# Kernel optimization log

Hardware: AMD Instinct MI355X
Metric: run time of the kernel (lower is better)

Reference implementation:

```python
import jax, jax.numpy as jnp
import numpy as np

N_NODES = 50000
N_EDGES = 800000
IN_DIM = 128
HID = 256
OUT_DIM = 256
N_HEADS = 8
E_DIM = 64
KV_IN = 2 * IN_DIM + E_DIM  # 320


def _mlp_params(key, din, dhid, dout):
    k1, k2 = jax.random.split(key)
    s1 = 1.0 / np.sqrt(din)
    s2 = 1.0 / np.sqrt(dhid)
    return (jax.random.uniform(k1, (din, dhid), jnp.float32, -s1, s1),
            jnp.zeros((dhid,), jnp.float32),
            jax.random.uniform(k2, (dhid, dout), jnp.float32, -s2, s2),
            jnp.zeros((dout,), jnp.float32))


def setup_inputs() -> dict:
    key = jax.random.key(0)
    kh, ke, kidx, kk, kv, kq = jax.random.split(key, 6)
    h = jax.random.normal(kh, (N_NODES, IN_DIM), jnp.float32)
    e = jax.random.normal(ke, (N_EDGES, E_DIM), jnp.float32)
    edge_index = jax.random.randint(kidx, (2, N_EDGES), 0, N_NODES, jnp.int64)
    Wk1, bk1, Wk2, bk2 = _mlp_params(kk, KV_IN, HID, OUT_DIM)
    Wv1, bv1, Wv2, bv2 = _mlp_params(kv, KV_IN, HID, OUT_DIM)
    Wq1, bq1, Wq2, bq2 = _mlp_params(kq, IN_DIM, HID, OUT_DIM)
    return {"h": h, "e": e, "edge_index": edge_index,
            "Wk1": Wk1, "bk1": bk1, "Wk2": Wk2, "bk2": bk2,
            "Wv1": Wv1, "bv1": bv1, "Wv2": Wv2, "bv2": bv2,
            "Wq1": Wq1, "bq1": bq1, "Wq2": Wq2, "bq2": bq2}


def _mlp(x, W1, b1, W2, b2):
    # MLP(in, out, hidden, norm=False): Linear -> ReLU -> Linear
    return jax.nn.relu(x @ W1 + b1) @ W2 + b2


def reference(h, e, edge_index,
              Wk1, bk1, Wk2, bk2,
              Wv1, bv1, Wv2, bv2,
              Wq1, bq1, Wq2, bq2):
    N = h.shape[0]
    d_head = OUT_DIM // N_HEADS
    src, dst = edge_index[0], edge_index[1]
    # gather endpoints: hi = h[dst], hj = h[src]
    kv_input = jnp.concatenate([e, h[dst], h[src]], axis=-1)  # [E, KV_IN]
    k = _mlp(kv_input, Wk1, bk1, Wk2, bk2).reshape(-1, N_HEADS, d_head)
    v = _mlp(kv_input, Wv1, bv1, Wv2, bv2).reshape(-1, N_HEADS, d_head)
    q = _mlp(h, Wq1, bq1, Wq2, bq2).reshape(-1, N_HEADS, d_head)
    # per-edge logits, scaled dot product [E, H]
    logits = jnp.sum(q[dst] * k, axis=-1) * (1.0 / np.sqrt(d_head))
    # scatter softmax over destination groups
    mx = jax.ops.segment_max(logits, dst, num_segments=N)  # [N, H]
    ex = jnp.exp(logits - mx[dst])
    den = jax.ops.segment_sum(ex, dst, num_segments=N)  # [N, H]
    alpha = ex / den[dst]  # [E, H]
    # weighted scatter-sum aggregate
    m = alpha[..., None] * v  # [E, H, d_head]
    out = jax.ops.segment_sum(m, dst, num_segments=N)  # [N, H, d_head]
    return out.reshape(N, OUT_DIM)
```

## Files before the change

### kernel.cpp

```cpp
#include <hip/hip_runtime.h>

#define NND 50000
#define NE  800000
#define IND 128
#define HD  256
#define OD  256
#define NH  8
#define ED  64
#define KVIN 320

typedef __attribute__((ext_vector_type(8))) short bf16x8;
typedef __attribute__((ext_vector_type(4))) float f32x4;

__device__ __forceinline__ float bf2f(unsigned short u) {
    union { unsigned int i; float f; } x; x.i = ((unsigned int)u) << 16; return x.f;
}
__device__ __forceinline__ unsigned short f2bf(float f) {
    union { float f; unsigned int i; } x; x.f = f;
    unsigned int u = x.i;
    u += 0x7FFFu + ((u >> 16) & 1u);
    return (unsigned short)(u >> 16);
}

__global__ void k_hist(const int* __restrict__ eidx, int* __restrict__ cnt) {
    int e = blockIdx.x * 256 + threadIdx.x;
    if (e < NE) atomicAdd(&cnt[eidx[NE + e]], 1);
}

__global__ __launch_bounds__(1024) void k_scan(const int* __restrict__ cnt,
                                               int* __restrict__ head) {
    __shared__ int part[1024];
    const int t = threadIdx.x;
    const int CH = (NND + 1023) / 1024;
    int base = t * CH;
    int s = 0;
    for (int i = 0; i < CH; ++i) { int idx = base + i; if (idx < NND) s += cnt[idx]; }
    part[t] = s;
    __syncthreads();
    for (int off = 1; off < 1024; off <<= 1) {
        int v = (t >= off) ? part[t - off] : 0;
        __syncthreads();
        part[t] += v;
        __syncthreads();
    }
    int excl = (t == 0) ? 0 : part[t - 1];
    for (int i = 0; i < CH; ++i) {
        int idx = base + i; if (idx >= NND) break;
        head[idx] = excl;
        excl += cnt[idx];
    }
}

__global__ void k_scatter(const int* __restrict__ eidx, int* __restrict__ head,
                          int* __restrict__ perm) {
    int e = blockIdx.x * 256 + threadIdx.x;
    if (e < NE) {
        int d = eidx[NE + e];
        int pos = atomicAdd(&head[d], 1);
        perm[pos] = e;
    }
}

__global__ void k_packw(const float* __restrict__ W, unsigned short* __restrict__ P,
                        int K, int N, int rowoff) {
    int tid = blockIdx.x * 256 + threadIdx.x;
    if (tid >= K * N) return;
    int j = tid & 7;
    int l = (tid >> 3) & 63;
    int rest = tid >> 9;
    int KS = K >> 5;
    int ks = rest % KS;
    int ct = rest / KS;
    int n = ct * 16 + (l & 15);
    int k = ks * 32 + (l >> 4) * 8 + j;
    P[tid] = f2bf(W[(size_t)(rowoff + k) * N + n]);
}

__global__ void k_h2bf(const float* __restrict__ h, unsigned short* __restrict__ hb, int n4) {
    int i = blockIdx.x * 256 + threadIdx.x;
    if (i < n4) {
        float4 v = *(const float4*)(h + (size_t)i * 4);
        ushort4 o;
        o.x = f2bf(v.x); o.y = f2bf(v.y); o.z = f2bf(v.z); o.w = f2bf(v.w);
        *(ushort4*)(hb + (size_t)i * 4) = o;
    }
}

__device__ __forceinline__ void zero_acc(f32x4 (&acc)[4][4]) {
    #pragma unroll
    for (int i = 0; i < 4; ++i)
        #pragma unroll
        for (int c = 0; c < 4; ++c)
            #pragma unroll
            for (int r = 0; r < 4; ++r) acc[i][c][r] = 0.f;
}

template<int KS, int STRIDE>
__device__ __forceinline__ void gemm_step(const unsigned short* A,
                                          const unsigned short* __restrict__ Wp,
                                          int w, int l, f32x4 (&acc)[4][4]) {
    for (int ks = 0; ks < KS; ++ks) {
        bf16x8 a[4], b[4];
        #pragma unroll
        for (int i = 0; i < 4; ++i)
            a[i] = *(const bf16x8*)(A + (i * 16 + (l & 15)) * STRIDE + ks * 32 + (l >> 4) * 8);
        #pragma unroll
        for (int c = 0; c < 4; ++c)
            b[c] = *(const bf16x8*)(Wp + (((4 * w + c) * KS + ks) * 64 + l) * 8);
        #pragma unroll
        for (int i = 0; i < 4; ++i)
            #pragma unroll
            for (int c = 0; c < 4; ++c)
                acc[i][c] = __builtin_amdgcn_mfma_f32_16x16x32_bf16(a[i], b[c], acc[i][c], 0, 0, 0);
    }
}

__global__ __launch_bounds__(256) void k_qmlp(
    const unsigned short* __restrict__ hb,
    const unsigned short* __restrict__ W1p, const float* __restrict__ b1,
    const unsigned short* __restrict__ W2p, const float* __restrict__ b2,
    unsigned short* __restrict__ qb)
{
    __shared__ unsigned short sX[64][136];
    __shared__ unsigned short sH[64][264];
    const int t = threadIdx.x, w = t >> 6, l = t & 63;
    const int m0 = blockIdx.x * 64;

    for (int c = t; c < 1024; c += 256) {
        int row = c >> 4, j = c & 15;
        int srcr = m0 + row; if (srcr >= NND) srcr = NND - 1;
        *(bf16x8*)(&sX[row][j * 8]) = *(const bf16x8*)(hb + (size_t)srcr * IND + j * 8);
    }
    __syncthreads();

    f32x4 acc[4][4];
    zero_acc(acc);
    gemm_step<4, 136>(&sX[0][0], W1p, w, l, acc);

    float bias1[4];
    #pragma unroll
    for (int c = 0; c < 4; ++c) bias1[c] = b1[64 * w + 16 * c + (l & 15)];
    #pragma unroll
    for (int i = 0; i < 4; ++i)
        #pragma unroll
        for (int c = 0; c < 4; ++c)
            #pragma unroll
            for (int r = 0; r < 4; ++r) {
                float v = acc[i][c][r] + bias1[c];
                v = v > 0.f ? v : 0.f;
                sH[i * 16 + (l >> 4) * 4 + r][64 * w + 16 * c + (l & 15)] = f2bf(v);
            }
    __syncthreads();

    zero_acc(acc);
    gemm_step<8, 264>(&sH[0][0], W2p, w, l, acc);

    float bias2[4];
    #pragma unroll
    for (int c = 0; c < 4; ++c) bias2[c] = b2[64 * w + 16 * c + (l & 15)];
    #pragma unroll
    for (int i = 0; i < 4; ++i)
        #pragma unroll
        for (int c = 0; c < 4; ++c)
            #pragma unroll
            for (int r = 0; r < 4; ++r) {
                int row = m0 + i * 16 + (l >> 4) * 4 + r;
                if (row < NND)
                    qb[(size_t)row * OD + 64 * w + 16 * c + (l & 15)] =
                        f2bf(acc[i][c][r] + bias2[c]);
            }
}

__global__ __launch_bounds__(256) void k_lin2(
    const unsigned short* __restrict__ hb,
    const unsigned short* __restrict__ Pd, const unsigned short* __restrict__ Ps,
    unsigned short* __restrict__ outd, unsigned short* __restrict__ outs)
{
    __shared__ unsigned short sX[64][136];
    const int t = threadIdx.x, w = t >> 6, l = t & 63;
    const int m0 = blockIdx.x * 64;

    for (int c = t; c < 1024; c += 256) {
        int row = c >> 4, j = c & 15;
        int srcr = m0 + row; if (srcr >= NND) srcr = NND - 1;
        *(bf16x8*)(&sX[row][j * 8]) = *(const bf16x8*)(hb + (size_t)srcr * IND + j * 8);
    }
    __syncthreads();

    f32x4 acc[4][4];
    zero_acc(acc);
    gemm_step<4, 136>(&sX[0][0], Pd, w, l, acc);
    #pragma unroll
    for (int i = 0; i < 4; ++i)
        #pragma unroll
        for (int c = 0; c < 4; ++c)
            #pragma unroll
            for (int r = 0; r < 4; ++r) {
                int row = m0 + i * 16 + (l >> 4) * 4 + r;
                if (row < NND)
                    outd[(size_t)row * HD + 64 * w + 16 * c + (l & 15)] = f2bf(acc[i][c][r]);
            }

    zero_acc(acc);
    gemm_step<4, 136>(&sX[0][0], Ps, w, l, acc);
    #pragma unroll
    for (int i = 0; i < 4; ++i)
        #pragma unroll
        for (int c = 0; c < 4; ++c)
            #pragma unroll
            for (int r = 0; r < 4; ++r) {
                int row = m0 + i * 16 + (l >> 4) * 4 + r;
                if (row < NND)
                    outs[(size_t)row * HD + 64 * w + 16 * c + (l & 15)] = f2bf(acc[i][c][r]);
            }
}

struct SmE {
    unsigned short E[64][72];
    unsigned short H[64][264];
    int   Eid[64];
    int   Src[64];
    int   Dst[64];
    float Ex[64][8];
};

__device__ __forceinline__ void stage_edges(SmE& sm, const float* __restrict__ eattr,
                                            const int* __restrict__ eidx,
                                            const int* __restrict__ perm,
                                            int e0, int t) {
    if (t < 64) {
        int eid = perm[e0 + t];
        sm.Eid[t] = eid;
        sm.Src[t] = eidx[eid];
        sm.Dst[t] = eidx[NE + eid];
    }
    __syncthreads();
    for (int c = t; c < 1024; c += 256) {
        int row = c >> 4, j = c & 15;
        float4 v = *(const float4*)(eattr + (size_t)sm.Eid[row] * ED + j * 4);
        ushort4 o; o.x = f2bf(v.x); o.y = f2bf(v.y); o.z = f2bf(v.z); o.w = f2bf(v.w);
        *(ushort4*)(&sm.E[row][j * 4]) = o;
    }
}

template<typename SM>
__device__ __forceinline__ void hidden_pass(SM& sm,
                                            const unsigned short* __restrict__ W1e,
                                            const float* __restrict__ b1,
                                            const unsigned short* __restrict__ ud,
                                            const unsigned short* __restrict__ us,
                                            int w, int l, int t, f32x4 (&acc)[4][4]) {
    zero_acc(acc);
    gemm_step<2, 72>(&sm.E[0][0], W1e, w, l, acc);
    float bias1[4];
    #pragma unroll
    for (int c = 0; c < 4; ++c) bias1[c] = b1[64 * w + 16 * c + (l & 15)];
    #pragma unroll
    for (int i = 0; i < 4; ++i)
        #pragma unroll
        for (int c = 0; c < 4; ++c)
            #pragma unroll
            for (int r = 0; r < 4; ++r)
                sm.H[i * 16 + (l >> 4) * 4 + r][64 * w + 16 * c + (l & 15)] =
                    f2bf(acc[i][c][r] + bias1[c]);
    __syncthreads();

    {
        int er = t >> 2;
        const unsigned short* udr = ud + (size_t)sm.Dst[er] * HD;
        const unsigned short* usr = us + (size_t)sm.Src[er] * HD;
        bf16x8 vd[8], vs[8];
        #pragma unroll
        for (int j = 0; j < 8; ++j) {
            int col = (j * 4 + (t & 3)) * 8;
            vd[j] = *(const bf16x8*)(udr + col);
            vs[j] = *(const bf16x8*)(usr + col);
        }
        #pragma unroll
        for (int j = 0; j < 8; ++j) {
            int col = (j * 4 + (t & 3)) * 8;
            bf16x8 hv = *(const bf16x8*)(&sm.H[er][col]);
            bf16x8 o;
            #pragma unroll
            for (int u = 0; u < 8; ++u) {
                float x = bf2f((unsigned short)hv[u]) + bf2f((unsigned short)vd[j][u])
                        + bf2f((unsigned short)vs[j][u]);
                o[u] = (short)f2bf(x > 0.f ? x : 0.f);
            }
            *(bf16x8*)(&sm.H[er][col]) = o;
        }
    }
    __syncthreads();
}

__global__ __launch_bounds__(256, 3) void k_edgeK(
    const float* __restrict__ eattr,
    const int* __restrict__ eidx, const int* __restrict__ perm,
    const unsigned short* __restrict__ W1e, const float* __restrict__ b1,
    const unsigned short* __restrict__ W2,  const float* __restrict__ b2,
    const unsigned short* __restrict__ ud,  const unsigned short* __restrict__ us,
    const unsigned short* __restrict__ qb,
    float* __restrict__ exbuf, float* __restrict__ den)
{
    __shared__ SmE sm;
    const int t = threadIdx.x, w = t >> 6, l = t & 63;
    const int e0 = blockIdx.x * 64;

    stage_edges(sm, eattr, eidx, perm, e0, t);
    __syncthreads();

    f32x4 acc[4][4];
    hidden_pass(sm, W1e, b1, ud, us, w, l, t, acc);

    zero_acc(acc);
    gemm_step<8, 264>(&sm.H[0][0], W2, w, l, acc);

    float bias2[4];
    #pragma unroll
    for (int c = 0; c < 4; ++c) bias2[c] = b2[64 * w + 16 * c + (l & 15)];
    __syncthreads();
    #pragma unroll
    for (int i = 0; i < 4; ++i)
        #pragma unroll
        for (int c = 0; c < 4; ++c)
            #pragma unroll
            for (int r = 0; r < 4; ++r)
                sm.H[i * 16 + (l >> 4) * 4 + r][64 * w + 16 * c + (l & 15)] =
                    f2bf(acc[i][c][r] + bias2[c]);
    __syncthreads();

    const float scale = 0.17677669529663687f;
    for (int p = t; p < 512; p += 256) {
        int er = p >> 3, hh = p & 7;
        int dn = sm.Dst[er];
        const unsigned short* qrow = qb + (size_t)dn * OD + hh * 32;
        float s = 0.f;
        #pragma unroll
        for (int jj = 0; jj < 32; jj += 8) {
            bf16x8 qv = *(const bf16x8*)(qrow + jj);
            bf16x8 kv = *(const bf16x8*)(&sm.H[er][hh * 32 + jj]);
            #pragma unroll
            for (int u = 0; u < 8; ++u)
                s += bf2f((unsigned short)qv[u]) * bf2f((unsigned short)kv[u]);
        }
        float ex = __expf(s * scale);
        exbuf[(size_t)(e0 + er) * NH + hh] = ex;
        sm.Ex[er][hh] = ex;
    }
    __syncthreads();
    if (t < NH) {
        float run = 0.f; int prev = sm.Dst[0];
        for (int er = 0; er < 64; ++er) {
            int dn = sm.Dst[er];
            if (dn != prev) { atomicAdd(&den[prev * NH + t], run); run = 0.f; prev = dn; }
            run += sm.Ex[er][t];
        }
        atomicAdd(&den[prev * NH + t], run);
    }
}

__global__ __launch_bounds__(256, 3) void k_edgeV(
    const float* __restrict__ eattr,
    const int* __restrict__ eidx, const int* __restrict__ perm,
    const unsigned short* __restrict__ W1e, const float* __restrict__ b1,
    const unsigned short* __restrict__ W2,  const float* __restrict__ b2,
    const unsigned short* __restrict__ ud,  const unsigned short* __restrict__ us,
    const float* __restrict__ exbuf, const float* __restrict__ den,
    float* __restrict__ outp)
{
    __shared__ SmE sm;
    const int t = threadIdx.x, w = t >> 6, l = t & 63;
    const int e0 = blockIdx.x * 64;

    stage_edges(sm, eattr, eidx, perm, e0, t);
    for (int p = t; p < 512; p += 256) {
        int er = p >> 3, hh = p & 7;
        sm.Ex[er][hh] = exbuf[(size_t)(e0 + er) * NH + hh] / den[sm.Dst[er] * NH + hh];
    }
    __syncthreads();

    f32x4 acc[4][4];
    hidden_pass(sm, W1e, b1, ud, us, w, l, t, acc);

    zero_acc(acc);
    gemm_step<8, 264>(&sm.H[0][0], W2, w, l, acc);

    float bias2[4];
    #pragma unroll
    for (int c = 0; c < 4; ++c) bias2[c] = b2[64 * w + 16 * c + (l & 15)];
    __syncthreads();
    #pragma unroll
    for (int i = 0; i < 4; ++i)
        #pragma unroll
        for (int c = 0; c < 4; ++c) {
            int col = 64 * w + 16 * c + (l & 15);
            int hh = col >> 5;
            #pragma unroll
            for (int r = 0; r < 4; ++r) {
                int er = i * 16 + (l >> 4) * 4 + r;
                sm.H[er][col] = f2bf((acc[i][c][r] + bias2[c]) * sm.Ex[er][hh]);
            }
        }
    __syncthreads();
    {
        float run = 0.f; int prev = sm.Dst[0];
        for (int er = 0; er < 64; ++er) {
            int dn = sm.Dst[er];
            if (dn != prev) {
                atomicAdd(outp + (size_t)prev * OD + t, run);
                run = 0.f; prev = dn;
            }
            run += bf2f(sm.H[er][t]);
        }
        atomicAdd(outp + (size_t)prev * OD + t, run);
    }
}

extern "C" void kernel_launch(void* const* d_in, const int* in_sizes, int n_in,
                              void* d_out, int out_size, void* d_ws, size_t ws_size,
                              hipStream_t stream)
{
    const float* h   = (const float*)d_in[0];
    const float* e   = (const float*)d_in[1];
    const int*   eid = (const int*)  d_in[2];
    const float* Wk1 = (const float*)d_in[3];
    const float* bk1 = (const float*)d_in[4];
    const float* Wk2 = (const float*)d_in[5];
    const float* bk2 = (const float*)d_in[6];
    const float* Wv1 = (const float*)d_in[7];
    const float* bv1 = (const float*)d_in[8];
    const float* Wv2 = (const float*)d_in[9];
    const float* bv2 = (const float*)d_in[10];
    const float* Wq1 = (const float*)d_in[11];
    const float* bq1 = (const float*)d_in[12];
    const float* Wq2 = (const float*)d_in[13];
    const float* bq2 = (const float*)d_in[14];

    char* ws = (char*)d_ws;
    unsigned short* hb   = (unsigned short*)(ws + 0);
    unsigned short* qb   = (unsigned short*)(ws + 12800000);
    unsigned short* udb  = (unsigned short*)(ws + 38400000);
    unsigned short* usb  = (unsigned short*)(ws + 64000000);
    float*          exb  = (float*)         (ws + 89600000);
    float*          den  = (float*)         (ws + 115200000);
    int*            cnt  = (int*)           (ws + 116800000);
    int*            head = (int*)           (ws + 117000000);
    int*            perm = (int*)           (ws + 117200000);
    unsigned short* Wq1p = (unsigned short*)(ws + 120400000);
    unsigned short* Wq2p = (unsigned short*)(ws + 120465536);
    unsigned short* WeK  = (unsigned short*)(ws + 120596608);
    unsigned short* W2K  = (unsigned short*)(ws + 120629376);
    unsigned short* WdK  = (unsigned short*)(ws + 120760448);
    unsigned short* WsK  = (unsigned short*)(ws + 120825984);
    unsigned short* WeV  = (unsigned short*)(ws + 120891520);
    unsigned short* W2V  = (unsigned short*)(ws + 120924288);
    unsigned short* WdV  = (unsigned short*)(ws + 121055360);
    unsigned short* WsV  = (unsigned short*)(ws + 121120896);
    const size_t needed = 121186432;
    if (ws_size < needed) return;

    hipMemsetAsync(d_out, 0, (size_t)NND * OD * sizeof(float), stream);
    hipMemsetAsync(den, 0, (size_t)NND * NH * sizeof(float), stream);
    hipMemsetAsync(cnt, 0, (size_t)NND * sizeof(int), stream);

    k_hist<<<(NE + 255) / 256, 256, 0, stream>>>(eid, cnt);
    k_scan<<<1, 1024, 0, stream>>>(cnt, head);
    k_scatter<<<(NE + 255) / 256, 256, 0, stream>>>(eid, head, perm);

    k_h2bf<<<(NND * IND / 4 + 255) / 256, 256, 0, stream>>>(h, hb, NND * IND / 4);

    k_packw<<<(IND * HD + 255) / 256, 256, 0, stream>>>(Wq1, Wq1p, IND, HD, 0);
    k_packw<<<(HD * OD + 255) / 256, 256, 0, stream>>>(Wq2, Wq2p, HD, OD, 0);
    k_packw<<<(ED * HD + 255) / 256, 256, 0, stream>>>(Wk1, WeK, ED, HD, 0);
    k_packw<<<(HD * OD + 255) / 256, 256, 0, stream>>>(Wk2, W2K, HD, OD, 0);
    k_packw<<<(IND * HD + 255) / 256, 256, 0, stream>>>(Wk1, WdK, IND, HD, 64);
    k_packw<<<(IND * HD + 255) / 256, 256, 0, stream>>>(Wk1, WsK, IND, HD, 192);
    k_packw<<<(ED * HD + 255) / 256, 256, 0, stream>>>(Wv1, WeV, ED, HD, 0);
    k_packw<<<(HD * OD + 255) / 256, 256, 0, stream>>>(Wv2, W2V, HD, OD, 0);
    k_packw<<<(IND * HD + 255) / 256, 256, 0, stream>>>(Wv1, WdV, IND, HD, 64);
    k_packw<<<(IND * HD + 255) / 256, 256, 0, stream>>>(Wv1, WsV, IND, HD, 192);

    k_qmlp<<<(NND + 63) / 64, 256, 0, stream>>>(hb, Wq1p, bq1, Wq2p, bq2, qb);

    k_lin2<<<(NND + 63) / 64, 256, 0, stream>>>(hb, WdK, WsK, udb, usb);
    k_edgeK<<<NE / 64, 256, 0, stream>>>(e, eid, perm, WeK, bk1, W2K, bk2,
                                         udb, usb, qb, exb, den);
    k_lin2<<<(NND + 63) / 64, 256, 0, stream>>>(hb, WdV, WsV, udb, usb);
    k_edgeV<<<NE / 64, 256, 0, stream>>>(e, eid, perm, WeV, bv1, W2V, bv2,
                                         udb, usb, exb, den, (float*)d_out);
}
```

Measured before the change: 921.7 us.

## Transpose MFMA operands so accumulators hold contiguous columns; fuse hidden epilogue gathers

Swaps the MFMA operand order so each lane's four accumulator values cover four consecutive output columns of one row. Epilogues can then pack bf16 pairs and use vector uint2 stores and float4 bias loads instead of scalar strided writes. The edge kernels' hidden layer no longer writes to shared memory, syncs, re-reads and adds the ud/us gathers in a separate pass. The gathered node projections are loaded straight into the first-layer epilogue registers, which removes one shared-memory round trip and one barrier. The cost is narrower global gathers (8-byte ushort4 per row instead of 16-byte bf16x8).

```diff
diff --git a/kernel.cpp b/kernel.cpp
--- a/kernel.cpp
+++ b/kernel.cpp
@@ -20,6 +20,9 @@
     unsigned int u = x.i;
     u += 0x7FFFu + ((u >> 16) & 1u);
     return (unsigned short)(u >> 16);
+}
+__device__ __forceinline__ unsigned int pk2(float a, float b) {
+    return (unsigned int)f2bf(a) | ((unsigned int)f2bf(b) << 16);
 }
 
 __global__ void k_hist(const int* __restrict__ eidx, int* __restrict__ cnt) {
@@ -88,30 +91,30 @@
 
 __device__ __forceinline__ void zero_acc(f32x4 (&acc)[4][4]) {
     #pragma unroll
-    for (int i = 0; i < 4; ++i)
+    for (int c = 0; c < 4; ++c)
+        #pragma unroll
+        for (int i = 0; i < 4; ++i)
+            #pragma unroll
+            for (int r = 0; r < 4; ++r) acc[c][i][r] = 0.f;
+}
+
+template<int KS, int STRIDE>
+__device__ __forceinline__ void gemmT(const unsigned short* X,
+                                      const unsigned short* __restrict__ Wp,
+                                      int w, int l, f32x4 (&acc)[4][4]) {
+    for (int ks = 0; ks < KS; ++ks) {
+        bf16x8 wf[4], xf[4];
+        #pragma unroll
+        for (int c = 0; c < 4; ++c)
+            wf[c] = *(const bf16x8*)(Wp + (((4 * w + c) * KS + ks) * 64 + l) * 8);
+        #pragma unroll
+        for (int i = 0; i < 4; ++i)
+            xf[i] = *(const bf16x8*)(X + (i * 16 + (l & 15)) * STRIDE + ks * 32 + (l >> 4) * 8);
         #pragma unroll
         for (int c = 0; c < 4; ++c)
             #pragma unroll
-            for (int r = 0; r < 4; ++r) acc[i][c][r] = 0.f;
-}
-
-template<int KS, int STRIDE>
-__device__ __forceinline__ void gemm_step(const unsigned short* A,
-                                          const unsigned short* __restrict__ Wp,
-                                          int w, int l, f32x4 (&acc)[4][4]) {
-    for (int ks = 0; ks < KS; ++ks) {
-        bf16x8 a[4], b[4];
-        #pragma unroll
-        for (int i = 0; i < 4; ++i)
-            a[i] = *(const bf16x8*)(A + (i * 16 + (l & 15)) * STRIDE + ks * 32 + (l >> 4) * 8);
-        #pragma unroll
-        for (int c = 0; c < 4; ++c)
-            b[c] = *(const bf16x8*)(Wp + (((4 * w + c) * KS + ks) * 64 + l) * 8);
-        #pragma unroll
-        for (int i = 0; i < 4; ++i)
-            #pragma unroll
-            for (int c = 0; c < 4; ++c)
-                acc[i][c] = __builtin_amdgcn_mfma_f32_16x16x32_bf16(a[i], b[c], acc[i][c], 0, 0, 0);
+            for (int i = 0; i < 4; ++i)
+                acc[c][i] = __builtin_amdgcn_mfma_f32_16x16x32_bf16(wf[c], xf[i], acc[c][i], 0, 0, 0);
     }
 }
 
@@ -124,6 +127,7 @@
     __shared__ unsigned short sX[64][136];
     __shared__ unsigned short sH[64][264];
     const int t = threadIdx.x, w = t >> 6, l = t & 63;
+    const int g = l >> 4, el = l & 15;
     const int m0 = blockIdx.x * 64;
 
     for (int c = t; c < 1024; c += 256) {
@@ -135,40 +139,43 @@
 
     f32x4 acc[4][4];
     zero_acc(acc);
-    gemm_step<4, 136>(&sX[0][0], W1p, w, l, acc);
-
-    float bias1[4];
-    #pragma unroll
-    for (int c = 0; c < 4; ++c) bias1[c] = b1[64 * w + 16 * c + (l & 15)];
-    #pragma unroll
-    for (int i = 0; i < 4; ++i)
-        #pragma unroll
-        for (int c = 0; c < 4; ++c)
-            #pragma unroll
-            for (int r = 0; r < 4; ++r) {
-                float v = acc[i][c][r] + bias1[c];
-                v = v > 0.f ? v : 0.f;
-                sH[i * 16 + (l >> 4) * 4 + r][64 * w + 16 * c + (l & 15)] = f2bf(v);
+    gemmT<4, 136>(&sX[0][0], W1p, w, l, acc);
+
+    #pragma unroll
+    for (int c = 0; c < 4; ++c) {
+        int hid0 = 64 * w + 16 * c + 4 * g;
+        float4 bv = *(const float4*)(b1 + hid0);
+        #pragma unroll
+        for (int i = 0; i < 4; ++i) {
+            int row = 16 * i + el;
+            float v0 = fmaxf(acc[c][i][0] + bv.x, 0.f);
+            float v1 = fmaxf(acc[c][i][1] + bv.y, 0.f);
+            float v2 = fmaxf(acc[c][i][2] + bv.z, 0.f);
+            float v3 = fmaxf(acc[c][i][3] + bv.w, 0.f);
+            uint2 pk; pk.x = pk2(v0, v1); pk.y = pk2(v2, v3);
+            *(uint2*)(&sH[row][hid0]) = pk;
+        }
+    }
+    __syncthreads();
+
+    zero_acc(acc);
+    gemmT<8, 264>(&sH[0][0], W2p, w, l, acc);
+
+    #pragma unroll
+    for (int c = 0; c < 4; ++c) {
+        int out0 = 64 * w + 16 * c + 4 * g;
+        float4 bv = *(const float4*)(b2 + out0);
+        #pragma unroll
+        for (int i = 0; i < 4; ++i) {
+            int node = m0 + 16 * i + el;
+            if (node < NND) {
+                uint2 pk;
+                pk.x = pk2(acc[c][i][0] + bv.x, acc[c][i][1] + bv.y);
+                pk.y = pk2(acc[c][i][2] + bv.z, acc[c][i][3] + bv.w);
+                *(uint2*)(qb + (size_t)node * OD + out0) = pk;
             }
-    __syncthreads();
-
-    zero_acc(acc);
-    gemm_step<8, 264>(&sH[0][0], W2p, w, l, acc);
-
-    float bias2[4];
-    #pragma unroll
-    for (int c = 0; c < 4; ++c) bias2[c] = b2[64 * w + 16 * c + (l & 15)];
-    #pragma unroll
-    for (int i = 0; i < 4; ++i)
-        #pragma unroll
-        for (int c = 0; c < 4; ++c)
-            #pragma unroll
-            for (int r = 0; r < 4; ++r) {
-                int row = m0 + i * 16 + (l >> 4) * 4 + r;
-                if (row < NND)
-                    qb[(size_t)row * OD + 64 * w + 16 * c + (l & 15)] =
-                        f2bf(acc[i][c][r] + bias2[c]);
-            }
+        }
+    }
 }
 
 __global__ __launch_bounds__(256) void k_lin2(
@@ -178,6 +185,7 @@
 {
     __shared__ unsigned short sX[64][136];
     const int t = threadIdx.x, w = t >> 6, l = t & 63;
+    const int g = l >> 4, el = l & 15;
     const int m0 = blockIdx.x * 64;
 
     for (int c = t; c < 1024; c += 256) {
@@ -189,30 +197,38 @@
 
     f32x4 acc[4][4];
     zero_acc(acc);
-    gemm_step<4, 136>(&sX[0][0], Pd, w, l, acc);
-    #pragma unroll
-    for (int i = 0; i < 4; ++i)
-        #pragma unroll
-        for (int c = 0; c < 4; ++c)
-            #pragma unroll
-            for (int r = 0; r < 4; ++r) {
-                int row = m0 + i * 16 + (l >> 4) * 4 + r;
-                if (row < NND)
-                    outd[(size_t)row * HD + 64 * w + 16 * c + (l & 15)] = f2bf(acc[i][c][r]);
+    gemmT<4, 136>(&sX[0][0], Pd, w, l, acc);
+    #pragma unroll
+    for (int c = 0; c < 4; ++c) {
+        int hid0 = 64 * w + 16 * c + 4 * g;
+        #pragma unroll
+        for (int i = 0; i < 4; ++i) {
+            int node = m0 + 16 * i + el;
+            if (node < NND) {
+                uint2 pk;
+                pk.x = pk2(acc[c][i][0], acc[c][i][1]);
+                pk.y = pk2(acc[c][i][2], acc[c][i][3]);
+                *(uint2*)(outd + (size_t)node * HD + hid0) = pk;
             }
-
-    zero_acc(acc);
-    gemm_step<4, 136>(&sX[0][0], Ps, w, l, acc);
-    #pragma unroll
-    for (int i = 0; i < 4; ++i)
-        #pragma unroll
-        for (int c = 0; c < 4; ++c)
-            #pragma unroll
-            for (int r = 0; r < 4; ++r) {
-                int row = m0 + i * 16 + (l >> 4) * 4 + r;
-                if (row < NND)
-                    outs[(size_t)row * HD + 64 * w + 16 * c + (l & 15)] = f2bf(acc[i][c][r]);
+        }
+    }
+
+    zero_acc(acc);
+    gemmT<4, 136>(&sX[0][0], Ps, w, l, acc);
+    #pragma unroll
+    for (int c = 0; c < 4; ++c) {
+        int hid0 = 64 * w + 16 * c + 4 * g;
+        #pragma unroll
+        for (int i = 0; i < 4; ++i) {
+            int node = m0 + 16 * i + el;
+            if (node < NND) {
+                uint2 pk;
+                pk.x = pk2(acc[c][i][0], acc[c][i][1]);
+                pk.y = pk2(acc[c][i][2], acc[c][i][3]);
+                *(uint2*)(outs + (size_t)node * HD + hid0) = pk;
             }
+        }
+    }
 }
 
 struct SmE {
@@ -243,54 +259,28 @@
     }
 }
 
-template<typename SM>
-__device__ __forceinline__ void hidden_pass(SM& sm,
-                                            const unsigned short* __restrict__ W1e,
-                                            const float* __restrict__ b1,
-                                            const unsigned short* __restrict__ ud,
-                                            const unsigned short* __restrict__ us,
-                                            int w, int l, int t, f32x4 (&acc)[4][4]) {
-    zero_acc(acc);
-    gemm_step<2, 72>(&sm.E[0][0], W1e, w, l, acc);
-    float bias1[4];
-    #pragma unroll
-    for (int c = 0; c < 4; ++c) bias1[c] = b1[64 * w + 16 * c + (l & 15)];
-    #pragma unroll
-    for (int i = 0; i < 4; ++i)
-        #pragma unroll
-        for (int c = 0; c < 4; ++c)
-            #pragma unroll
-            for (int r = 0; r < 4; ++r)
-                sm.H[i * 16 + (l >> 4) * 4 + r][64 * w + 16 * c + (l & 15)] =
-                    f2bf(acc[i][c][r] + bias1[c]);
-    __syncthreads();
-
-    {
-        int er = t >> 2;
-        const unsigned short* udr = ud + (size_t)sm.Dst[er] * HD;
-        const unsigned short* usr = us + (size_t)sm.Src[er] * HD;
-        bf16x8 vd[8], vs[8];
-        #pragma unroll
-        for (int j = 0; j < 8; ++j) {
-            int col = (j * 4 + (t & 3)) * 8;
-            vd[j] = *(const bf16x8*)(udr + col);
-            vs[j] = *(const bf16x8*)(usr + col);
-        }
-        #pragma unroll
-        for (int j = 0; j < 8; ++j) {
-            int col = (j * 4 + (t & 3)) * 8;
-            bf16x8 hv = *(const bf16x8*)(&sm.H[er][col]);
-            bf16x8 o;
-            #pragma unroll
-            for (int u = 0; u < 8; ++u) {
-                float x = bf2f((unsigned short)hv[u]) + bf2f((unsigned short)vd[j][u])
-                        + bf2f((unsigned short)vs[j][u]);
-                o[u] = (short)f2bf(x > 0.f ? x : 0.f);
-            }
-            *(bf16x8*)(&sm.H[er][col]) = o;
-        }
-    }
-    __syncthreads();
+__device__ __forceinline__ void hidden_epi(SmE& sm, f32x4 (&acc)[4][4],
+                                           const float* __restrict__ b1,
+                                           const unsigned short* __restrict__ ud,
+                                           const unsigned short* __restrict__ us,
+                                           const int (&dstE)[4], const int (&srcE)[4],
+                                           int w, int g, int el) {
+    #pragma unroll
+    for (int c = 0; c < 4; ++c) {
+        int hid0 = 64 * w + 16 * c + 4 * g;
+        float4 bv = *(const float4*)(b1 + hid0);
+        #pragma unroll
+        for (int i = 0; i < 4; ++i) {
+            ushort4 u4 = *(const ushort4*)(ud + (size_t)dstE[i] * HD + hid0);
+            ushort4 s4 = *(const ushort4*)(us + (size_t)srcE[i] * HD + hid0);
+            float v0 = fmaxf(acc[c][i][0] + bv.x + bf2f(u4.x) + bf2f(s4.x), 0.f);
+            float v1 = fmaxf(acc[c][i][1] + bv.y + bf2f(u4.y) + bf2f(s4.y), 0.f);
+            float v2 = fmaxf(acc[c][i][2] + bv.z + bf2f(u4.z) + bf2f(s4.z), 0.f);
+            float v3 = fmaxf(acc[c][i][3] + bv.w + bf2f(u4.w) + bf2f(s4.w), 0.f);
+            uint2 pk; pk.x = pk2(v0, v1); pk.y = pk2(v2, v3);
+            *(uint2*)(&sm.H[16 * i + el][hid0]) = pk;
+        }
+    }
 }
 
 __global__ __launch_bounds__(256, 3) void k_edgeK(
@@ -304,29 +294,38 @@
 {
     __shared__ SmE sm;
     const int t = threadIdx.x, w = t >> 6, l = t & 63;
+    const int g = l >> 4, el = l & 15;
     const int e0 = blockIdx.x * 64;
 
     stage_edges(sm, eattr, eidx, perm, e0, t);
     __syncthreads();
 
+    int dstE[4], srcE[4];
+    #pragma unroll
+    for (int i = 0; i < 4; ++i) { dstE[i] = sm.Dst[16 * i + el]; srcE[i] = sm.Src[16 * i + el]; }
+
     f32x4 acc[4][4];
-    hidden_pass(sm, W1e, b1, ud, us, w, l, t, acc);
-
-    zero_acc(acc);
-    gemm_step<8, 264>(&sm.H[0][0], W2, w, l, acc);
-
-    float bias2[4];
-    #pragma unroll
-    for (int c = 0; c < 4; ++c) bias2[c] = b2[64 * w + 16 * c + (l & 15)];
-    __syncthreads();
-    #pragma unroll
-    for (int i = 0; i < 4; ++i)
-        #pragma unroll
-        for (int c = 0; c < 4; ++c)
-            #pragma unroll
-            for (int r = 0; r < 4; ++r)
-                sm.H[i * 16 + (l >> 4) * 4 + r][64 * w + 16 * c + (l & 15)] =
-                    f2bf(acc[i][c][r] + bias2[c]);
+    zero_acc(acc);
+    gemmT<2, 72>(&sm.E[0][0], W1e, w, l, acc);
+    hidden_epi(sm, acc, b1, ud, us, dstE, srcE, w, g, el);
+    __syncthreads();
+
+    zero_acc(acc);
+    gemmT<8, 264>(&sm.H[0][0], W2, w, l, acc);
+    __syncthreads();
+
+    #pragma unroll
+    for (int c = 0; c < 4; ++c) {
+        int out0 = 64 * w + 16 * c + 4 * g;
+        float4 bv = *(const float4*)(b2 + out0);
+        #pragma unroll
+        for (int i = 0; i < 4; ++i) {
+            uint2 pk;
+            pk.x = pk2(acc[c][i][0] + bv.x, acc[c][i][1] + bv.y);
+            pk.y = pk2(acc[c][i][2] + bv.z, acc[c][i][3] + bv.w);
+            *(uint2*)(&sm.H[16 * i + el][out0]) = pk;
+        }
+    }
     __syncthreads();
 
     const float scale = 0.17677669529663687f;
@@ -370,6 +369,7 @@
 {
     __shared__ SmE sm;
     const int t = threadIdx.x, w = t >> 6, l = t & 63;
+    const int g = l >> 4, el = l & 15;
     const int e0 = blockIdx.x * 64;
 
     stage_edges(sm, eattr, eidx, perm, e0, t);
@@ -379,28 +379,35 @@
     }
     __syncthreads();
 
+    int dstE[4], srcE[4];
+    #pragma unroll
+    for (int i = 0; i < 4; ++i) { dstE[i] = sm.Dst[16 * i + el]; srcE[i] = sm.Src[16 * i + el]; }
+
     f32x4 acc[4][4];
-    hidden_pass(sm, W1e, b1, ud, us, w, l, t, acc);
-
-    zero_acc(acc);
-    gemm_step<8, 264>(&sm.H[0][0], W2, w, l, acc);
-
-    float bias2[4];
-    #pragma unroll
-    for (int c = 0; c < 4; ++c) bias2[c] = b2[64 * w + 16 * c + (l & 15)];
-    __syncthreads();
-    #pragma unroll
-    for (int i = 0; i < 4; ++i)
-        #pragma unroll
-        for (int c = 0; c < 4; ++c) {
-            int col = 64 * w + 16 * c + (l & 15);
-            int hh = col >> 5;
-            #pragma unroll
-            for (int r = 0; r < 4; ++r) {
-                int er = i * 16 + (l >> 4) * 4 + r;
-                sm.H[er][col] = f2bf((acc[i][c][r] + bias2[c]) * sm.Ex[er][hh]);
-            }
-        }
+    zero_acc(acc);
+    gemmT<2, 72>(&sm.E[0][0], W1e, w, l, acc);
+    hidden_epi(sm, acc, b1, ud, us, dstE, srcE, w, g, el);
+    __syncthreads();
+
+    zero_acc(acc);
+    gemmT<8, 264>(&sm.H[0][0], W2, w, l, acc);
+    __syncthreads();
+
+    #pragma unroll
+    for (int c = 0; c < 4; ++c) {
+        int out0 = 64 * w + 16 * c + 4 * g;
+        float4 bv = *(const float4*)(b2 + out0);
+        int hh = out0 >> 5;
+        #pragma unroll
+        for (int i = 0; i < 4; ++i) {
+            int edge = 16 * i + el;
+            float al = sm.Ex[edge][hh];
+            uint2 pk;
+            pk.x = pk2((acc[c][i][0] + bv.x) * al, (acc[c][i][1] + bv.y) * al);
+            pk.y = pk2((acc[c][i][2] + bv.z) * al, (acc[c][i][3] + bv.w) * al);
+            *(uint2*)(&sm.H[edge][out0]) = pk;
+        }
+    }
     __syncthreads();
     {
         float run = 0.f; int prev = sm.Dst[0];
```

New measurement: 1.069 ms. 1.16x slower.
